# Kernel optimization log

Measured on AMD Instinct MI355X. Metric: run time of the kernel, lower is better.

Reference implementation:

```python
import jax, jax.numpy as jnp
import numpy as np

B, S, D, H, HD = 2, 4096, 768, 12, 64
W = 256  # one-sided attention window (attention_window=512 // 2)
SCALE = 1.0 / np.sqrt(HD).astype(np.float32)
NEG = -1e9


def setup_inputs() -> dict:
    key = jax.random.key(0)
    ks = jax.random.split(key, 13)
    inp = {"hidden_states": jax.random.normal(ks[0], (B, S, D), dtype=jnp.float32)}
    names = ["Wq", "Wk", "Wv", "Wqg", "Wkg", "Wvg"]
    for i, n in enumerate(names):
        inp[n] = jax.random.normal(ks[1 + i], (D, D), dtype=jnp.float32) * 0.02
        inp["b" + n[1:]] = jax.random.normal(ks[7 + i], (D,), dtype=jnp.float32) * 0.02
    inp["num_global"] = 32
    return inp


def _heads(x):
    # [B,S,D] -> [B,H,S,HD]
    return x.reshape(B, S, H, HD).transpose(0, 2, 1, 3)


def longformer_attn(hidden_states, Wq, bq, Wk, bk, Wv, bv, Wqg, bqg, Wkg, bkg, Wvg, bvg, G):
    q = _heads(hidden_states @ Wq + bq) * SCALE
    k = _heads(hidden_states @ Wk + bk)
    v = _heads(hidden_states @ Wv + bv)

    nc = S // W  # number of query chunks
    # --- banded (sliding window) scores via overlapping key chunks of size 3W ---
    Qc = q.reshape(B, H, nc, W, HD)
    kpad = jnp.pad(k, ((0, 0), (0, 0), (W, W), (0, 0)))
    win_idx = jnp.arange(nc)[:, None] * W + jnp.arange(3 * W)[None, :]  # [nc, 3W]
    K3 = kpad[:, :, win_idx]  # [B,H,nc,3W,HD]
    band = jnp.einsum('bhcqd,bhckd->bhcqk', Qc, K3)  # [B,H,nc,W,3W]
    # mask: key abs position in range, and relative offset within [-W, W]
    c = jnp.arange(nc)[:, None, None]
    pq = jnp.arange(W)[None, :, None]
    e = jnp.arange(3 * W)[None, None, :]
    kabs = c * W + e - W
    valid = (kabs >= 0) & (kabs < S) & (e >= pq) & (e <= pq + 2 * W)
    band = jnp.where(valid[None, None], band, NEG).reshape(B, H, S, 3 * W)

    # --- all queries also attend to the G global keys (regular key proj) ---
    sg = jnp.einsum('bhsd,bhgd->bhsg', q, k[:, :, :G])  # [B,H,S,G]
    probs = jax.nn.softmax(jnp.concatenate([sg, band], axis=-1), axis=-1)
    pg, pb = probs[..., :G], probs[..., G:].reshape(B, H, nc, W, 3 * W)

    vpad = jnp.pad(v, ((0, 0), (0, 0), (W, W), (0, 0)))
    V3 = vpad[:, :, win_idx]  # [B,H,nc,3W,HD]
    out = jnp.einsum('bhcqk,bhckd->bhcqd', pb, V3).reshape(B, H, S, HD)
    out = out + jnp.einsum('bhsg,bhgd->bhsd', pg, v[:, :, :G])

    # --- global queries attend to ALL tokens with the *_global projections ---
    qg = _heads(hidden_states @ Wqg + bqg)[:, :, :G] * SCALE  # [B,H,G,HD]
    kgf = _heads(hidden_states @ Wkg + bkg)
    vgf = _heads(hidden_states @ Wvg + bvg)
    gp = jax.nn.softmax(jnp.einsum('bhgd,bhsd->bhgs', qg, kgf), axis=-1)
    gout = jnp.einsum('bhgs,bhsd->bhgd', gp, vgf)  # [B,H,G,HD]
    out = out.at[:, :, :G].set(gout)

    return out.transpose(0, 2, 1, 3).reshape(B, S, D)


def reference(hidden_states, Wq, bq, Wk, bk, Wv, bv, Wqg, bqg, Wkg, bkg, Wvg, bvg, num_global):
    return longformer_attn(hidden_states, Wq, bq, Wk, bk, Wv, bv, Wqg, bqg, Wkg, bkg, Wvg, bvg, int(num_global))
```

## Files before the change

kernel.cpp:

```cpp
#include <hip/hip_runtime.h>
#include <hip/hip_bf16.h>


#define DEVI __device__ __forceinline__
typedef _Float16 f16;
typedef _Float16 h4 __attribute__((ext_vector_type(4)));
typedef _Float16 f16x8 __attribute__((ext_vector_type(8)));
typedef __attribute__((ext_vector_type(4))) float float4v;

DEVI float4v mfma16(f16x8 a, f16x8 b, float4v c) {
    return __builtin_amdgcn_mfma_f32_16x16x32_f16(a, b, c, 0, 0, 0);
}

DEVI void gl_lds16(const f16* g, f16* l) {
    __builtin_amdgcn_global_load_lds(
        (const __attribute__((address_space(1))) unsigned int*)g,
        (__attribute__((address_space(3))) unsigned int*)l, 16, 0, 0);
}

__global__ __launch_bounds__(256) void xcast(const float* __restrict__ x,
                                             f16* __restrict__ xh) {
    int i = (blockIdx.x * 256 + threadIdx.x) * 4;
    float4 v = *(const float4*)&x[i];
    h4 o = {(f16)v.x, (f16)v.y, (f16)v.z, (f16)v.w};
    *(h4*)&xh[i] = o;
}

__global__ __launch_bounds__(256) void wprep(
    const float* __restrict__ w0, const float* __restrict__ w1,
    const float* __restrict__ w2, const float* __restrict__ w3,
    const float* __restrict__ w4, const float* __restrict__ w5,
    f16* __restrict__ wt) {
    __shared__ float tile[64][65];
    int i = blockIdx.z;
    const float* W = (i == 0) ? w0 : (i == 1) ? w1 : (i == 2) ? w2
                   : (i == 3) ? w3 : (i == 4) ? w4 : w5;
    int n0 = blockIdx.x * 64, k0 = blockIdx.y * 64;
    int tx = threadIdx.x & 63, ty = threadIdx.x >> 6;
#pragma unroll
    for (int yy = 0; yy < 64; yy += 4)
        tile[yy + ty][tx] = W[(size_t)(k0 + yy + ty) * 768 + n0 + tx];
    __syncthreads();
#pragma unroll
    for (int yy = 0; yy < 64; yy += 4)
        wt[(size_t)(i * 768 + n0 + yy + ty) * 768 + k0 + tx] = (f16)tile[tx][yy + ty];
}

__global__ __launch_bounds__(256) void qkv_mfma3(
    const f16* __restrict__ Xh, const f16* __restrict__ Wt,
    const float* __restrict__ b0, const float* __restrict__ b1,
    const float* __restrict__ b2, const float* __restrict__ b3,
    const float* __restrict__ b4, const float* __restrict__ b5,
    f16* __restrict__ q, f16* __restrict__ k, f16* __restrict__ vT,
    f16* __restrict__ qg, f16* __restrict__ kg, f16* __restrict__ vgT) {
    constexpr int CLD = 136;
    __shared__ __align__(16) f16 At[128 * 32];
    __shared__ __align__(16) f16 Bt[128 * 32];
    __shared__ __align__(16) f16 Cl[128 * CLD];
    int tid = threadIdx.x, lane = tid & 63, wid = tid >> 6;
    int quad = lane >> 4, l15 = lane & 15;
    int m0 = blockIdx.x * 128;
    int wm = (wid >> 1) * 64, wn = (wid & 1) * 64;
    const f16* arow0 = Xh + (size_t)m0 * 768;
    const f16* brow0 = Wt + (size_t)blockIdx.y * 128 * 768;

    float4v acc[4][4];
#pragma unroll
    for (int mt = 0; mt < 4; ++mt)
#pragma unroll
        for (int nt = 0; nt < 4; ++nt) acc[mt][nt] = (float4v){0.f, 0.f, 0.f, 0.f};

    int s0 = tid, s1 = tid + 256;
    int r0 = s0 >> 2, o0 = (s0 & 3) * 8;
    int r1 = s1 >> 2, o1 = (s1 & 3) * 8;
    f16* ldsA0 = &At[wid * 512];
    f16* ldsB0 = &Bt[wid * 512];
    f16* ldsA1 = &At[2048 + wid * 512];
    f16* ldsB1 = &Bt[2048 + wid * 512];
    for (int kt = 0; kt < 24; ++kt) {
        int k0 = kt * 32;
        __syncthreads();
        gl_lds16(&arow0[(size_t)r0 * 768 + k0 + o0], ldsA0);
        gl_lds16(&brow0[(size_t)r0 * 768 + k0 + o0], ldsB0);
        gl_lds16(&arow0[(size_t)r1 * 768 + k0 + o1], ldsA1);
        gl_lds16(&brow0[(size_t)r1 * 768 + k0 + o1], ldsB1);
        __syncthreads();
        f16x8 af[4], bf[4];
#pragma unroll
        for (int mt = 0; mt < 4; ++mt)
            af[mt] = *(const f16x8*)&At[(wm + mt * 16 + l15) * 32 + quad * 8];
#pragma unroll
        for (int nt = 0; nt < 4; ++nt)
            bf[nt] = *(const f16x8*)&Bt[(wn + nt * 16 + l15) * 32 + quad * 8];
#pragma unroll
        for (int mt = 0; mt < 4; ++mt)
#pragma unroll
            for (int nt = 0; nt < 4; ++nt) acc[mt][nt] = mfma16(af[mt], bf[nt], acc[mt][nt]);
    }

    int grp = blockIdx.y / 6;
    const float* Bsel = (grp == 0) ? b0 : (grp == 1) ? b1 : (grp == 2) ? b2
                      : (grp == 3) ? b3 : (grp == 4) ? b4 : b5;
    int nb = (blockIdx.y - grp * 6) * 128;
    int b = m0 >> 12;
    bool tr = (grp == 2 || grp == 5);

    if (tr) {
#pragma unroll
        for (int nt = 0; nt < 4; ++nt) {
            float bias = Bsel[nb + wn + nt * 16 + l15];
#pragma unroll
            for (int mt = 0; mt < 4; ++mt) {
                float4v a = acc[mt][nt];
                h4 pk = {(f16)(a[0] + bias), (f16)(a[1] + bias),
                         (f16)(a[2] + bias), (f16)(a[3] + bias)};
                *(h4*)&Cl[(wn + nt * 16 + l15) * CLD + wm + mt * 16 + quad * 4] = pk;
            }
        }
    } else {
        float scale = (grp == 0 || grp == 3) ? 0.125f : 1.0f;
#pragma unroll
        for (int nt = 0; nt < 4; ++nt) {
            float bias = Bsel[nb + wn + nt * 16 + l15];
#pragma unroll
            for (int mt = 0; mt < 4; ++mt) {
                float4v a = acc[mt][nt];
#pragma unroll
                for (int r = 0; r < 4; ++r)
                    Cl[(wm + mt * 16 + quad * 4 + r) * CLD + wn + nt * 16 + l15] =
                        (f16)((a[r] + bias) * scale);
            }
        }
    }
    __syncthreads();

    if (tr) {
        f16* base = (grp == 2) ? vT : vgT;
        int c = tid & 127, sh = (tid >> 7) * 64;
        int ncol = nb + c, h = ncol >> 6, hd = ncol & 63;
        f16* dst = &base[((size_t)((b * 12 + h) * 64 + hd)) * 4096 + (m0 & 4095) + sh];
        const f16* src = &Cl[c * CLD + sh];
#pragma unroll
        for (int i = 0; i < 8; ++i)
            *(f16x8*)&dst[i * 8] = *(const f16x8*)&src[i * 8];
    } else {
        int sl = tid & 127, hh = tid >> 7;
        int s = (m0 & 4095) + sl;
        int h = (nb + hh * 64) >> 6;
        const f16* src = &Cl[sl * CLD + hh * 64];
        f16* dst = nullptr;
        if (grp == 3) {
            if (s < 32) dst = &qg[((size_t)((b * 12 + h) * 32 + s)) * 64];
        } else {
            f16* baseb = (grp == 0) ? q : (grp == 1) ? k : kg;
            dst = &baseb[((size_t)((b * 12 + h) * 4096 + s)) * 64];
        }
        if (dst)
#pragma unroll
            for (int i = 0; i < 8; ++i)
                *(f16x8*)&dst[i * 8] = *(const f16x8*)&src[i * 8];
    }
}

__global__ __launch_bounds__(256, 3) void band_mfma4(
    const f16* __restrict__ q, const f16* __restrict__ k, const f16* __restrict__ vT,
    float* __restrict__ out) {
    constexpr int LDK = 72;
    constexpr int LDP = 40;
    __shared__ __align__(16) f16 Kt[64 * LDK];
    __shared__ __align__(16) f16 Vt[64 * LDK];
    __shared__ __align__(16) f16 Pt[4][32 * LDP];
    int tid = threadIdx.x, lane = tid & 63, wid = tid >> 6;
    int quad = lane >> 4, l15 = lane & 15;
    int c = blockIdx.x & 31, h = (blockIdx.x >> 5) % 12, b = blockIdx.x / 384;
    const f16* qsl = q + (size_t)(b * 12 + h) * 4096 * 64;
    const f16* ksl = k + (size_t)(b * 12 + h) * 4096 * 64;
    const f16* vsl = vT + (size_t)(b * 12 + h) * 64 * 4096;
    int q0 = c * 128;
    int pq0 = q0 + wid * 32;

    f16x8 qf[2][2];
#pragma unroll
    for (int qg = 0; qg < 2; ++qg)
#pragma unroll
        for (int ks = 0; ks < 2; ++ks)
            qf[qg][ks] = *(const f16x8*)&qsl[(size_t)(pq0 + qg * 16 + l15) * 64 +
                                             ks * 32 + quad * 8];

    float4v Ot[4][2];
#pragma unroll
    for (int dt = 0; dt < 4; ++dt)
#pragma unroll
        for (int qg = 0; qg < 2; ++qg) Ot[dt][qg] = (float4v){0.f, 0.f, 0.f, 0.f};
    float lacc[2] = {0.f, 0.f};
    f16* PW = &Pt[wid][0];

    for (int t = 0; t < 11; ++t) {
        int kb = 0;
        if (t != 0) {
            kb = q0 - 256 + (t - 1) * 64;
            if (kb < 0 || kb >= 4096) continue;
        }
        __syncthreads();
        {
            int r = tid >> 2, o = (tid & 3) * 16;
            f16x8 ka = *(const f16x8*)&ksl[(size_t)(kb + r) * 64 + o];
            f16x8 kb2 = *(const f16x8*)&ksl[(size_t)(kb + r) * 64 + o + 8];
            f16x8 va = *(const f16x8*)&vsl[(size_t)r * 4096 + kb + o];
            f16x8 vb2 = *(const f16x8*)&vsl[(size_t)r * 4096 + kb + o + 8];
            *(f16x8*)&Kt[r * LDK + o] = ka;
            *(f16x8*)&Kt[r * LDK + o + 8] = kb2;
            *(f16x8*)&Vt[r * LDK + o] = va;
            *(f16x8*)&Vt[r * LDK + o + 8] = vb2;
        }
        __syncthreads();

        if (t != 0 && (kb + 63 < pq0 - 256 || kb > pq0 + 31 + 256)) continue;

        int nh = (t == 0) ? 1 : 2;
        for (int hf = 0; hf < nh; ++hf) {
#pragma unroll
            for (int jt = 0; jt < 2; ++jt) {
                int jl = hf * 32 + jt * 16;
                f16x8 kf0 = *(const f16x8*)&Kt[(jl + l15) * LDK + quad * 8];
                f16x8 kf1 = *(const f16x8*)&Kt[(jl + l15) * LDK + 32 + quad * 8];
                int j0 = kb + jl;
#pragma unroll
                for (int qg = 0; qg < 2; ++qg) {
                    int qlo = pq0 + qg * 16;
                    h4 pk = {(f16)0.f, (f16)0.f, (f16)0.f, (f16)0.f};
                    bool dead = (t != 0) && ((j0 < qlo - 271) || (j0 > qlo + 271));
                    if (!dead) {
                        float4v sacc = (float4v){0.f, 0.f, 0.f, 0.f};
                        sacc = mfma16(kf0, qf[qg][0], sacc);
                        sacc = mfma16(kf1, qf[qg][1], sacc);
                        float p[4];
                        bool full = (t == 0) || ((j0 >= qlo - 241) && (j0 <= qlo + 241));
                        if (full) {
#pragma unroll
                            for (int r = 0; r < 4; ++r) p[r] = __expf(sacc[r]);
                        } else {
#pragma unroll
                            for (int r = 0; r < 4; ++r) {
                                int d = (j0 + quad * 4 + r) - (qlo + l15);
                                p[r] = ((unsigned)(d + 256) <= 512u) ? __expf(sacc[r]) : 0.f;
                            }
                        }
                        lacc[qg] += (p[0] + p[1]) + (p[2] + p[3]);
                        pk = (h4){(f16)p[0], (f16)p[1], (f16)p[2], (f16)p[3]};
                    }
                    *(h4*)&PW[(qg * 16 + l15) * LDP + jt * 16 + quad * 4] = pk;
                }
            }
            asm volatile("s_waitcnt lgkmcnt(0)" ::: "memory");
            f16x8 pf0 = *(const f16x8*)&PW[l15 * LDP + quad * 8];
            f16x8 pf1 = *(const f16x8*)&PW[(16 + l15) * LDP + quad * 8];
#pragma unroll
            for (int dt = 0; dt < 4; ++dt) {
                f16x8 vf = *(const f16x8*)&Vt[(dt * 16 + l15) * LDK + hf * 32 + quad * 8];
                Ot[dt][0] = mfma16(vf, pf0, Ot[dt][0]);
                Ot[dt][1] = mfma16(vf, pf1, Ot[dt][1]);
            }
        }
    }

#pragma unroll
    for (int qg = 0; qg < 2; ++qg) {
        float lsum = lacc[qg];
        lsum += __shfl_xor(lsum, 16);
        lsum += __shfl_xor(lsum, 32);
        float inv = 1.f / lsum;
        size_t orow = (size_t)(b * 4096 + pq0 + qg * 16 + l15) * 768 + h * 64;
#pragma unroll
        for (int dt = 0; dt < 4; ++dt) {
            float4 o4 = {Ot[dt][qg][0] * inv, Ot[dt][qg][1] * inv,
                         Ot[dt][qg][2] * inv, Ot[dt][qg][3] * inv};
            *(float4*)&out[orow + dt * 16 + quad * 4] = o4;
        }
    }
}

__global__ __launch_bounds__(256) void global_part(
    const f16* __restrict__ qg, const f16* __restrict__ kg, const f16* __restrict__ vgT,
    float* __restrict__ Opart, float* __restrict__ Lpart) {
    constexpr int LDP = 72;
    __shared__ __align__(16) f16 Pt[4][32 * LDP];
    __shared__ __align__(16) float Osh[4][64 * 32];
    __shared__ float Lsh[4][32];
    int tid = threadIdx.x, lane = tid & 63, wid = tid >> 6;
    int quad = lane >> 4, l15 = lane & 15;
    int sl = blockIdx.x & 7, bh = blockIdx.x >> 3;
    const f16* qsl = qg + (size_t)bh * 32 * 64;
    const f16* ksl = kg + (size_t)bh * 4096 * 64;
    const f16* vsl = vgT + (size_t)bh * 64 * 4096;
    int kbase = sl * 512 + wid * 128;

    f16x8 qf[2][2];
#pragma unroll
    for (int g = 0; g < 2; ++g)
#pragma unroll
        for (int ks = 0; ks < 2; ++ks)
            qf[g][ks] = *(const f16x8*)&qsl[(size_t)(g * 16 + l15) * 64 + ks * 32 + quad * 8];

    float4v Ot[4][2];
#pragma unroll
    for (int dt = 0; dt < 4; ++dt)
#pragma unroll
        for (int g = 0; g < 2; ++g) Ot[dt][g] = (float4v){0.f, 0.f, 0.f, 0.f};
    float lacc[2] = {0.f, 0.f};
    f16* PW = &Pt[wid][0];

#pragma unroll
    for (int hf = 0; hf < 2; ++hf) {
        int kh0 = kbase + hf * 64;
#pragma unroll
        for (int kt = 0; kt < 4; ++kt) {
            int jb = kh0 + kt * 16;
            f16x8 kf0 = *(const f16x8*)&ksl[(size_t)(jb + l15) * 64 + quad * 8];
            f16x8 kf1 = *(const f16x8*)&ksl[(size_t)(jb + l15) * 64 + 32 + quad * 8];
#pragma unroll
            for (int g = 0; g < 2; ++g) {
                float4v sacc = (float4v){0.f, 0.f, 0.f, 0.f};
                sacc = mfma16(kf0, qf[g][0], sacc);
                sacc = mfma16(kf1, qf[g][1], sacc);
                float p0 = __expf(sacc[0]), p1 = __expf(sacc[1]);
                float p2 = __expf(sacc[2]), p3 = __expf(sacc[3]);
                lacc[g] += (p0 + p1) + (p2 + p3);
                h4 pk = {(f16)p0, (f16)p1, (f16)p2, (f16)p3};
                *(h4*)&PW[(g * 16 + l15) * LDP + kt * 16 + quad * 4] = pk;
            }
        }
        asm volatile("s_waitcnt lgkmcnt(0)" ::: "memory");
#pragma unroll
        for (int kh = 0; kh < 2; ++kh) {
            f16x8 pf0 = *(const f16x8*)&PW[l15 * LDP + kh * 32 + quad * 8];
            f16x8 pf1 = *(const f16x8*)&PW[(16 + l15) * LDP + kh * 32 + quad * 8];
#pragma unroll
            for (int dt = 0; dt < 4; ++dt) {
                f16x8 vf = *(const f16x8*)&vsl[(size_t)(dt * 16 + l15) * 4096 +
                                               kh0 + kh * 32 + quad * 8];
                Ot[dt][0] = mfma16(vf, pf0, Ot[dt][0]);
                Ot[dt][1] = mfma16(vf, pf1, Ot[dt][1]);
            }
        }
    }

#pragma unroll
    for (int g = 0; g < 2; ++g) {
        lacc[g] += __shfl_xor(lacc[g], 16);
        lacc[g] += __shfl_xor(lacc[g], 32);
    }
    if (quad == 0) { Lsh[wid][l15] = lacc[0]; Lsh[wid][16 + l15] = lacc[1]; }
#pragma unroll
    for (int dt = 0; dt < 4; ++dt)
#pragma unroll
        for (int g = 0; g < 2; ++g)
#pragma unroll
            for (int r = 0; r < 4; ++r)
                Osh[wid][(dt * 16 + quad * 4 + r) * 32 + g * 16 + l15] = Ot[dt][g][r];
    __syncthreads();
#pragma unroll
    for (int i = 0; i < 8; ++i) {
        int idx = tid + i * 256;
        int d = idx & 63, qq = idx >> 6;
        float v = Osh[0][d * 32 + qq] + Osh[1][d * 32 + qq] +
                  Osh[2][d * 32 + qq] + Osh[3][d * 32 + qq];
        Opart[(size_t)blockIdx.x * 2048 + idx] = v;
    }
    if (tid < 32)
        Lpart[blockIdx.x * 32 + tid] = Lsh[0][tid] + Lsh[1][tid] + Lsh[2][tid] + Lsh[3][tid];
}

__global__ __launch_bounds__(256) void global_reduce(
    const float* __restrict__ Opart, const float* __restrict__ Lpart,
    float* __restrict__ out) {
    __shared__ float Ls[32];
    int tid = threadIdx.x, bh = blockIdx.x;
    int b = bh / 12, h = bh % 12;
    if (tid < 32) {
        float s = 0.f;
#pragma unroll
        for (int sl = 0; sl < 8; ++sl) s += Lpart[(bh * 8 + sl) * 32 + tid];
        Ls[tid] = s;
    }
    __syncthreads();
#pragma unroll
    for (int i = 0; i < 8; ++i) {
        int idx = tid + i * 256;
        int d = idx & 63, qq = idx >> 6;
        float o = 0.f;
#pragma unroll
        for (int sl = 0; sl < 8; ++sl) o += Opart[(size_t)(bh * 8 + sl) * 2048 + idx];
        out[(size_t)(b * 4096 + qq) * 768 + h * 64 + d] = o / Ls[qq];
    }
}

extern "C" void kernel_launch(void* const* d_in, const int* in_sizes, int n_in,
                              void* d_out, int out_size, void* d_ws, size_t ws_size,
                              hipStream_t stream) {
    const float* hs = (const float*)d_in[0];
    float* outp = (float*)d_out;

    char* p = (char*)d_ws;
    const size_t SLAB = (size_t)2 * 12 * 4096 * 64 * sizeof(f16);
    f16* qb   = (f16*)(p + 0 * SLAB);
    f16* kb   = (f16*)(p + 1 * SLAB);
    f16* vtb  = (f16*)(p + 2 * SLAB);
    f16* kgb  = (f16*)(p + 3 * SLAB);
    f16* vgtb = (f16*)(p + 4 * SLAB);
    f16* qgb  = (f16*)(p + 5 * SLAB);
    char* p2  = p + 5 * SLAB + 196608;
    f16* xh   = (f16*)p2;
    f16* wt   = (f16*)(p2 + SLAB);
    char* p3  = p2 + SLAB + 7077888;
    float* Opart = (float*)p3;
    float* Lpart = (float*)(p3 + 1572864);

    xcast<<<6144, 256, 0, stream>>>(hs, xh);
    wprep<<<dim3(12, 12, 6), 256, 0, stream>>>(
        (const float*)d_in[1], (const float*)d_in[3], (const float*)d_in[5],
        (const float*)d_in[7], (const float*)d_in[9], (const float*)d_in[11], wt);
    qkv_mfma3<<<dim3(64, 36), 256, 0, stream>>>(
        xh, wt,
        (const float*)d_in[2], (const float*)d_in[4], (const float*)d_in[6],
        (const float*)d_in[8], (const float*)d_in[10], (const float*)d_in[12],
        qb, kb, vtb, qgb, kgb, vgtb);
    band_mfma4<<<768, 256, 0, stream>>>(qb, kb, vtb, outp);
    global_part<<<192, 256, 0, stream>>>(qgb, kgb, vgtb, Opart, Lpart);
    global_reduce<<<24, 256, 0, stream>>>(Opart, Lpart, outp);
}
```

Baseline: 238.8 us.

## Stage 128-key tiles in band kernel and read global keys directly

The banded attention kernel now stages 128-key K/V tiles per loop iteration instead of 64, which halves the number of block-wide barriers and load rounds. The global-key block (the first 32 keys) is computed straight from global memory before the main loop, so it no longer takes a shared-memory staging pass. Explicit lgkmcnt waits before reading the per-wave P scratch are removed, which relies on the compiler inserting the needed waits. The larger LDS footprint may lower occupancy below the requested three blocks per CU.

```diff
diff --git a/kernel.cpp b/kernel.cpp
--- a/kernel.cpp
+++ b/kernel.cpp
@@ -162,13 +162,12 @@
     }
 }
 
-__global__ __launch_bounds__(256, 3) void band_mfma4(
+__global__ __launch_bounds__(256, 3) void band_mfma5(
     const f16* __restrict__ q, const f16* __restrict__ k, const f16* __restrict__ vT,
     float* __restrict__ out) {
-    constexpr int LDK = 72;
-    constexpr int LDP = 40;
-    __shared__ __align__(16) f16 Kt[64 * LDK];
-    __shared__ __align__(16) f16 Vt[64 * LDK];
+    constexpr int LDK = 72, LDV = 136, LDP = 40;
+    __shared__ __align__(16) f16 Kt[128 * LDK];
+    __shared__ __align__(16) f16 Vt[64 * LDV];
     __shared__ __align__(16) f16 Pt[4][32 * LDP];
     int tid = threadIdx.x, lane = tid & 63, wid = tid >> 6;
     int quad = lane >> 4, l15 = lane & 15;
@@ -195,71 +194,101 @@
     float lacc[2] = {0.f, 0.f};
     f16* PW = &Pt[wid][0];
 
-    for (int t = 0; t < 11; ++t) {
-        int kb = 0;
-        if (t != 0) {
-            kb = q0 - 256 + (t - 1) * 64;
-            if (kb < 0 || kb >= 4096) continue;
-        }
+    {
+#pragma unroll
+        for (int jt = 0; jt < 2; ++jt) {
+            f16x8 kf0 = *(const f16x8*)&ksl[(size_t)(jt * 16 + l15) * 64 + quad * 8];
+            f16x8 kf1 = *(const f16x8*)&ksl[(size_t)(jt * 16 + l15) * 64 + 32 + quad * 8];
+#pragma unroll
+            for (int qg = 0; qg < 2; ++qg) {
+                float4v sacc = (float4v){0.f, 0.f, 0.f, 0.f};
+                sacc = mfma16(kf0, qf[qg][0], sacc);
+                sacc = mfma16(kf1, qf[qg][1], sacc);
+                float p0 = __expf(sacc[0]), p1 = __expf(sacc[1]);
+                float p2 = __expf(sacc[2]), p3 = __expf(sacc[3]);
+                lacc[qg] += (p0 + p1) + (p2 + p3);
+                h4 pk = {(f16)p0, (f16)p1, (f16)p2, (f16)p3};
+                *(h4*)&PW[(qg * 16 + l15) * LDP + jt * 16 + quad * 4] = pk;
+            }
+        }
+        f16x8 pf0 = *(const f16x8*)&PW[l15 * LDP + quad * 8];
+        f16x8 pf1 = *(const f16x8*)&PW[(16 + l15) * LDP + quad * 8];
+#pragma unroll
+        for (int dt = 0; dt < 4; ++dt) {
+            f16x8 vf = *(const f16x8*)&vsl[(size_t)(dt * 16 + l15) * 4096 + quad * 8];
+            Ot[dt][0] = mfma16(vf, pf0, Ot[dt][0]);
+            Ot[dt][1] = mfma16(vf, pf1, Ot[dt][1]);
+        }
+    }
+
+    for (int r = 0; r < 5; ++r) {
+        int kb = q0 - 256 + r * 128;
+        if (kb < 0 || kb >= 4096) continue;
         __syncthreads();
         {
-            int r = tid >> 2, o = (tid & 3) * 16;
-            f16x8 ka = *(const f16x8*)&ksl[(size_t)(kb + r) * 64 + o];
-            f16x8 kb2 = *(const f16x8*)&ksl[(size_t)(kb + r) * 64 + o + 8];
-            f16x8 va = *(const f16x8*)&vsl[(size_t)r * 4096 + kb + o];
-            f16x8 vb2 = *(const f16x8*)&vsl[(size_t)r * 4096 + kb + o + 8];
-            *(f16x8*)&Kt[r * LDK + o] = ka;
-            *(f16x8*)&Kt[r * LDK + o + 8] = kb2;
-            *(f16x8*)&Vt[r * LDK + o] = va;
-            *(f16x8*)&Vt[r * LDK + o + 8] = vb2;
+            int kr = tid >> 1, ko = (tid & 1) * 32;
+            const f16* ks2 = &ksl[(size_t)(kb + kr) * 64 + ko];
+            f16* kd = &Kt[kr * LDK + ko];
+#pragma unroll
+            for (int i = 0; i < 4; ++i) *(f16x8*)&kd[i * 8] = *(const f16x8*)&ks2[i * 8];
+            int vr = tid >> 2, vo = (tid & 3) * 32;
+            const f16* vs2 = &vsl[(size_t)vr * 4096 + kb + vo];
+            f16* vd = &Vt[vr * LDV + vo];
+#pragma unroll
+            for (int i = 0; i < 4; ++i) *(f16x8*)&vd[i * 8] = *(const f16x8*)&vs2[i * 8];
         }
         __syncthreads();
 
-        if (t != 0 && (kb + 63 < pq0 - 256 || kb > pq0 + 31 + 256)) continue;
-
-        int nh = (t == 0) ? 1 : 2;
-        for (int hf = 0; hf < nh; ++hf) {
-#pragma unroll
-            for (int jt = 0; jt < 2; ++jt) {
-                int jl = hf * 32 + jt * 16;
-                f16x8 kf0 = *(const f16x8*)&Kt[(jl + l15) * LDK + quad * 8];
-                f16x8 kf1 = *(const f16x8*)&Kt[(jl + l15) * LDK + 32 + quad * 8];
-                int j0 = kb + jl;
-#pragma unroll
-                for (int qg = 0; qg < 2; ++qg) {
-                    int qlo = pq0 + qg * 16;
-                    h4 pk = {(f16)0.f, (f16)0.f, (f16)0.f, (f16)0.f};
-                    bool dead = (t != 0) && ((j0 < qlo - 271) || (j0 > qlo + 271));
-                    if (!dead) {
-                        float4v sacc = (float4v){0.f, 0.f, 0.f, 0.f};
-                        sacc = mfma16(kf0, qf[qg][0], sacc);
-                        sacc = mfma16(kf1, qf[qg][1], sacc);
-                        float p[4];
-                        bool full = (t == 0) || ((j0 >= qlo - 241) && (j0 <= qlo + 241));
-                        if (full) {
-#pragma unroll
-                            for (int r = 0; r < 4; ++r) p[r] = __expf(sacc[r]);
-                        } else {
-#pragma unroll
-                            for (int r = 0; r < 4; ++r) {
-                                int d = (j0 + quad * 4 + r) - (qlo + l15);
-                                p[r] = ((unsigned)(d + 256) <= 512u) ? __expf(sacc[r]) : 0.f;
+        if (kb + 127 < pq0 - 256 || kb > pq0 + 287) continue;
+
+#pragma unroll
+        for (int tt = 0; tt < 2; ++tt) {
+            int tb = kb + tt * 64;
+            if (tb + 63 < pq0 - 256 || tb > pq0 + 287) continue;
+#pragma unroll
+            for (int hf = 0; hf < 2; ++hf) {
+#pragma unroll
+                for (int jt = 0; jt < 2; ++jt) {
+                    int jl = tt * 64 + hf * 32 + jt * 16;
+                    f16x8 kf0 = *(const f16x8*)&Kt[(jl + l15) * LDK + quad * 8];
+                    f16x8 kf1 = *(const f16x8*)&Kt[(jl + l15) * LDK + 32 + quad * 8];
+                    int j0 = kb + jl;
+#pragma unroll
+                    for (int qg = 0; qg < 2; ++qg) {
+                        int qlo = pq0 + qg * 16;
+                        h4 pk = {(f16)0.f, (f16)0.f, (f16)0.f, (f16)0.f};
+                        bool dead = (j0 < qlo - 271) || (j0 > qlo + 271);
+                        if (!dead) {
+                            float4v sacc = (float4v){0.f, 0.f, 0.f, 0.f};
+                            sacc = mfma16(kf0, qf[qg][0], sacc);
+                            sacc = mfma16(kf1, qf[qg][1], sacc);
+                            float p[4];
+                            bool full = (j0 >= qlo - 241) && (j0 <= qlo + 241);
+                            if (full) {
+#pragma unroll
+                                for (int rr = 0; rr < 4; ++rr) p[rr] = __expf(sacc[rr]);
+                            } else {
+#pragma unroll
+                                for (int rr = 0; rr < 4; ++rr) {
+                                    int d = (j0 + quad * 4 + rr) - (qlo + l15);
+                                    p[rr] = ((unsigned)(d + 256) <= 512u) ? __expf(sacc[rr]) : 0.f;
+                                }
                             }
+                            lacc[qg] += (p[0] + p[1]) + (p[2] + p[3]);
+                            pk = (h4){(f16)p[0], (f16)p[1], (f16)p[2], (f16)p[3]};
                         }
-                        lacc[qg] += (p[0] + p[1]) + (p[2] + p[3]);
-                        pk = (h4){(f16)p[0], (f16)p[1], (f16)p[2], (f16)p[3]};
+                        *(h4*)&PW[(qg * 16 + l15) * LDP + jt * 16 + quad * 4] = pk;
                     }
-                    *(h4*)&PW[(qg * 16 + l15) * LDP + jt * 16 + quad * 4] = pk;
                 }
-            }
-            asm volatile("s_waitcnt lgkmcnt(0)" ::: "memory");
-            f16x8 pf0 = *(const f16x8*)&PW[l15 * LDP + quad * 8];
-            f16x8 pf1 = *(const f16x8*)&PW[(16 + l15) * LDP + quad * 8];
-#pragma unroll
-            for (int dt = 0; dt < 4; ++dt) {
-                f16x8 vf = *(const f16x8*)&Vt[(dt * 16 + l15) * LDK + hf * 32 + quad * 8];
-                Ot[dt][0] = mfma16(vf, pf0, Ot[dt][0]);
-                Ot[dt][1] = mfma16(vf, pf1, Ot[dt][1]);
+                f16x8 pf0 = *(const f16x8*)&PW[l15 * LDP + quad * 8];
+                f16x8 pf1 = *(const f16x8*)&PW[(16 + l15) * LDP + quad * 8];
+#pragma unroll
+                for (int dt = 0; dt < 4; ++dt) {
+                    f16x8 vf = *(const f16x8*)&Vt[(dt * 16 + l15) * LDV +
+                                                  tt * 64 + hf * 32 + quad * 8];
+                    Ot[dt][0] = mfma16(vf, pf0, Ot[dt][0]);
+                    Ot[dt][1] = mfma16(vf, pf1, Ot[dt][1]);
+                }
             }
         }
     }
@@ -330,7 +359,6 @@
                 *(h4*)&PW[(g * 16 + l15) * LDP + kt * 16 + quad * 4] = pk;
             }
         }
-        asm volatile("s_waitcnt lgkmcnt(0)" ::: "memory");
 #pragma unroll
         for (int kh = 0; kh < 2; ++kh) {
             f16x8 pf0 = *(const f16x8*)&PW[l15 * LDP + kh * 32 + quad * 8];
@@ -425,7 +453,7 @@
         (const float*)d_in[2], (const float*)d_in[4], (const float*)d_in[6],
         (const float*)d_in[8], (const float*)d_in[10], (const float*)d_in[12],
         qb, kb, vtb, qgb, kgb, vgtb);
-    band_mfma4<<<768, 256, 0, stream>>>(qb, kb, vtb, outp);
+    band_mfma5<<<768, 256, 0, stream>>>(qb, kb, vtb, outp);
     global_part<<<192, 256, 0, stream>>>(qgb, kgb, vgtb, Opart, Lpart);
     global_reduce<<<24, 256, 0, stream>>>(Opart, Lpart, outp);
 }
```

Result: no change. 236.1 us (-1.1%).
